# Kernel optimization log

Hardware: AMD Instinct MI355X
Metric: run time of the kernel (lower is better)

The kernel has to match this reference:

```python
import jax, jax.numpy as jnp
import numpy as np

B, H, N, P = 2, 8, 2048, 64   # batch, heads, seq, head_dim
M, D = 4, 256                 # sketch count, sketch feature dim


def setup_inputs() -> dict:
    key = jax.random.key(0)
    kq, kk, ks, kr = jax.random.split(key, 4)
    scale = P ** -0.5  # keep exp(QK) numerically tame, std(dot) ~= 1/8
    Q = jax.random.normal(kq, (B, H, N, P), dtype=jnp.float32) * scale
    K = jax.random.normal(kk, (B, H, N, P), dtype=jnp.float32) * scale
    # indices into the concatenated [Q;K] token axis of length 2N
    sketching_matrix = jax.random.randint(ks, (B, M, D), 0, 2 * N)
    # Rademacher random signs, broadcast over [b,h,2n] in the reduction
    random_sign = jnp.sign(jax.random.normal(kr, (M, D), dtype=jnp.float32))
    random_sign = jnp.where(random_sign == 0, 1.0, random_sign)
    return {"Q": Q, "K": K, "sketching_matrix": sketching_matrix,
            "random_sign": random_sign}


def reference(Q, K, sketching_matrix, random_sign):
    b, h, n, p = Q.shape
    X = jnp.concatenate([Q, K], axis=2)          # [b,h,2n,p]
    Xt = jnp.transpose(X, (0, 2, 1, 3))          # [b,2n,h,p]
    # gather sketched landmarks: [b,m,d,h,p] -> [b,h,m,d,p]
    XS = Xt[jnp.arange(b)[:, None, None], sketching_matrix]
    XS = jnp.transpose(XS, (0, 3, 1, 2, 4))
    # RS_SM accumulate branch: exp of inner products, random-sign reduce over m
    product = jnp.einsum('bhnp,bhmdp->bhnmd', X, XS)   # [b,h,2n,m,d]
    AS = jnp.einsum('bhnmd,md->bhnd', jnp.exp(product), random_sign)
    return AS.astype(Q.dtype)                    # [b,h,2n,d]
```

## Files before the change

### kernel.cpp

```cpp
#include <hip/hip_runtime.h>
#include <hip/hip_bf16.h>

typedef __attribute__((ext_vector_type(8))) short short8;
typedef __attribute__((ext_vector_type(4))) float f32x4;

namespace {
constexpr int Hc  = 8;
constexpr int Nc  = 2048;
constexpr int NXc = 4096;
constexpr int Pc  = 64;
constexpr int Mc  = 4;
constexpr int Dc  = 256;
constexpr int TN  = 128;
constexpr int LDX = 72;
constexpr int DCk = 64;
}

__device__ inline unsigned int bfpack(float a, float b) {
  union { __hip_bfloat162 h; unsigned int u; } cv;
  cv.h = __float22bfloat162_rn(make_float2(a, b));
  return cv.u;
}

__global__ __launch_bounds__(256, 2) void sketch_kernel(
    const float* __restrict__ Q, const float* __restrict__ K,
    const int* __restrict__ SK, const float* __restrict__ SGN,
    float* __restrict__ OUT)
{
  __shared__ __hip_bfloat16 Xs[TN][LDX];
  __shared__ __hip_bfloat16 Ws[DCk][LDX];
  __shared__ float Ss[Mc * Dc];

  const int t    = threadIdx.x;
  const int lane = t & 63;
  const int wv   = t >> 6;
  const int bh   = blockIdx.y;
  const int b    = bh >> 3;
  const int n0   = blockIdx.x * TN;

  for (int i = t; i < Mc * Dc; i += 256) Ss[i] = SGN[i];

  {
    const int q  = t & 3;
    const int r0 = t >> 2;
    for (int half = 0; half < 2; ++half) {
      const int r = r0 + half * 64;
      const int n = n0 + r;
      const float* src = (n < Nc) ? (Q + ((size_t)bh * Nc + n) * Pc)
                                  : (K + ((size_t)bh * Nc + (n - Nc)) * Pc);
      const f32x4* s4 = (const f32x4*)(src + q * 16);
      f32x4 f0 = s4[0], f1 = s4[1], f2 = s4[2], f3 = s4[3];
      uint4 u, v;
      u.x = bfpack(f0.x, f0.y); u.y = bfpack(f0.z, f0.w);
      u.z = bfpack(f1.x, f1.y); u.w = bfpack(f1.z, f1.w);
      v.x = bfpack(f2.x, f2.y); v.y = bfpack(f2.z, f2.w);
      v.z = bfpack(f3.x, f3.y); v.w = bfpack(f3.z, f3.w);
      *(uint4*)&Xs[r][q * 16]     = u;
      *(uint4*)&Xs[r][q * 16 + 8] = v;
    }
  }

  __syncthreads();

  short8 afr[2][2];
  const int acol = (lane >> 4) * 8;
  {
    const int arow = wv * 32 + (lane & 15);
    for (int ti = 0; ti < 2; ++ti)
      for (int ks = 0; ks < 2; ++ks)
        afr[ti][ks] = *(const short8*)&Xs[arow + ti * 16][ks * 32 + acol];
  }

  for (int dc = 0; dc < 4; ++dc) {
    f32x4 AS[2][4];
    for (int ti = 0; ti < 2; ++ti)
      for (int tj = 0; tj < 4; ++tj)
        AS[ti][tj] = (f32x4){0.f, 0.f, 0.f, 0.f};

    for (int m = 0; m < Mc; ++m) {
      __syncthreads();
      {
        const int q = t & 3;
        const int r = t >> 2;
        const int d = dc * 64 + r;
        const int idx = SK[b * (Mc * Dc) + m * Dc + d];
        const float* src = (idx < Nc) ? (Q + ((size_t)bh * Nc + idx) * Pc)
                                      : (K + ((size_t)bh * Nc + (idx - Nc)) * Pc);
        const f32x4* s4 = (const f32x4*)(src + q * 16);
        f32x4 f0 = s4[0], f1 = s4[1], f2 = s4[2], f3 = s4[3];
        uint4 u, v;
        u.x = bfpack(f0.x, f0.y); u.y = bfpack(f0.z, f0.w);
        u.z = bfpack(f1.x, f1.y); u.w = bfpack(f1.z, f1.w);
        v.x = bfpack(f2.x, f2.y); v.y = bfpack(f2.z, f2.w);
        v.z = bfpack(f3.x, f3.y); v.w = bfpack(f3.z, f3.w);
        *(uint4*)&Ws[r][q * 16]     = u;
        *(uint4*)&Ws[r][q * 16 + 8] = v;
      }
      __syncthreads();

      short8 bfr[4][2];
      const int brow = lane & 15;
      for (int tj = 0; tj < 4; ++tj)
        for (int ks = 0; ks < 2; ++ks)
          bfr[tj][ks] = *(const short8*)&Ws[tj * 16 + brow][ks * 32 + acol];

      for (int ti = 0; ti < 2; ++ti)
        for (int tj = 0; tj < 4; ++tj) {
          f32x4 c = {0.f, 0.f, 0.f, 0.f};
          c = __builtin_amdgcn_mfma_f32_16x16x32_bf16(afr[ti][0], bfr[tj][0], c, 0, 0, 0);
          c = __builtin_amdgcn_mfma_f32_16x16x32_bf16(afr[ti][1], bfr[tj][1], c, 0, 0, 0);
          const float sg = Ss[m * Dc + dc * 64 + tj * 16 + (lane & 15)];
          AS[ti][tj].x += sg * __expf(c.x);
          AS[ti][tj].y += sg * __expf(c.y);
          AS[ti][tj].z += sg * __expf(c.z);
          AS[ti][tj].w += sg * __expf(c.w);
        }
    }

    const int dbase = dc * 64 + (lane & 15);
    const int nb    = n0 + wv * 32 + ((lane >> 4) << 2);
    for (int ti = 0; ti < 2; ++ti)
      for (int tj = 0; tj < 4; ++tj) {
        const size_t base = ((size_t)bh * NXc + (nb + ti * 16)) * Dc + dbase + tj * 16;
        OUT[base + 0 * (size_t)Dc] = AS[ti][tj].x;
        OUT[base + 1 * (size_t)Dc] = AS[ti][tj].y;
        OUT[base + 2 * (size_t)Dc] = AS[ti][tj].z;
        OUT[base + 3 * (size_t)Dc] = AS[ti][tj].w;
      }
  }
}

extern "C" void kernel_launch(void* const* d_in, const int* in_sizes, int n_in,
                              void* d_out, int out_size, void* d_ws, size_t ws_size,
                              hipStream_t stream) {
  (void)in_sizes; (void)n_in; (void)out_size; (void)d_ws; (void)ws_size;
  const float* Q   = (const float*)d_in[0];
  const float* K   = (const float*)d_in[1];
  const int*   SK  = (const int*)d_in[2];
  const float* SGN = (const float*)d_in[3];
  float* OUT = (float*)d_out;

  dim3 grid(NXc / TN, 16);
  dim3 block(256);
  sketch_kernel<<<grid, block, 0, stream>>>(Q, K, SK, SGN, OUT);
}
```

Measured before the change: 105.0 us.

## Split into bf16 prepass plus double-buffered MFMA main kernel with exp2

A prepass kernel converts Q/K rows and the gathered sketch landmarks to bf16 once into workspace, folding log2(e) into the landmark rows so the main kernel can use a hardware exp2. This removes the repeated fp32 gather and convert work each block did before. The main kernel uses smaller 64-row tiles for more blocks and higher occupancy, double-buffers the landmark tile in shared memory with register prefetch, and walks a flattened 16-step (dc, m) loop. It adds a second launch and a workspace round-trip, and scaling before the bf16 rounding slightly changes the numerics.

Result: faster. 102.3 us (-2.6%).

```diff
diff --git a/kernel.cpp b/kernel.cpp
--- a/kernel.cpp
+++ b/kernel.cpp
@@ -5,15 +5,22 @@
 typedef __attribute__((ext_vector_type(4))) float f32x4;
 
 namespace {
-constexpr int Hc  = 8;
 constexpr int Nc  = 2048;
 constexpr int NXc = 4096;
 constexpr int Pc  = 64;
 constexpr int Mc  = 4;
 constexpr int Dc  = 256;
-constexpr int TN  = 128;
-constexpr int LDX = 72;
-constexpr int DCk = 64;
+constexpr int BH  = 16;
+constexpr int LDW = 72;
+constexpr float LOG2E = 1.4426950408889634f;
+}
+
+__device__ inline float fexp2(float x) {
+#if __has_builtin(__builtin_amdgcn_exp2f)
+  return __builtin_amdgcn_exp2f(x);
+#else
+  return exp2f(x);
+#endif
 }
 
 __device__ inline unsigned int bfpack(float a, float b) {
@@ -22,125 +29,146 @@
   return cv.u;
 }
 
-__global__ __launch_bounds__(256, 2) void sketch_kernel(
+__global__ __launch_bounds__(256) void prepass_kernel(
     const float* __restrict__ Q, const float* __restrict__ K,
-    const int* __restrict__ SK, const float* __restrict__ SGN,
-    float* __restrict__ OUT)
+    const int* __restrict__ SK,
+    __hip_bfloat16* __restrict__ Xb, __hip_bfloat16* __restrict__ Wb)
 {
-  __shared__ __hip_bfloat16 Xs[TN][LDX];
-  __shared__ __hip_bfloat16 Ws[DCk][LDX];
+  const int t = blockIdx.x * 256 + threadIdx.x;
+  const int q = t & 7;
+  const int r = t >> 3;
+  const int NXROWS = BH * NXc;
+
+  const float* src;
+  __hip_bfloat16* dst;
+  float scale;
+  if (r < NXROWS) {
+    const int bh = r >> 12, n = r & (NXc - 1);
+    src = (n < Nc) ? (Q + ((size_t)bh * Nc + n) * Pc)
+                   : (K + ((size_t)bh * Nc + (n - Nc)) * Pc);
+    dst = Xb + (size_t)r * Pc;
+    scale = 1.0f;
+  } else {
+    const int j  = r - NXROWS;
+    const int bh = j >> 10;
+    const int md = j & 1023;
+    const int b  = bh >> 3;
+    const int idx = SK[b * (Mc * Dc) + md];
+    src = (idx < Nc) ? (Q + ((size_t)bh * Nc + idx) * Pc)
+                     : (K + ((size_t)bh * Nc + (idx - Nc)) * Pc);
+    dst = Wb + (size_t)j * Pc;
+    scale = LOG2E;
+  }
+  const f32x4* s4 = (const f32x4*)(src + q * 8);
+  f32x4 f0 = s4[0], f1 = s4[1];
+  uint4 u;
+  u.x = bfpack(f0.x * scale, f0.y * scale);
+  u.y = bfpack(f0.z * scale, f0.w * scale);
+  u.z = bfpack(f1.x * scale, f1.y * scale);
+  u.w = bfpack(f1.z * scale, f1.w * scale);
+  *(uint4*)(dst + q * 8) = u;
+}
+
+__global__ __launch_bounds__(256, 4) void sketch_main(
+    const __hip_bfloat16* __restrict__ Xb, const __hip_bfloat16* __restrict__ Wb,
+    const float* __restrict__ SGN, float* __restrict__ OUT)
+{
+  __shared__ __hip_bfloat16 Ws[2][64][LDW];
   __shared__ float Ss[Mc * Dc];
 
   const int t    = threadIdx.x;
   const int lane = t & 63;
   const int wv   = t >> 6;
   const int bh   = blockIdx.y;
-  const int b    = bh >> 3;
-  const int n0   = blockIdx.x * TN;
+  const int n0   = blockIdx.x * 64;
 
   for (int i = t; i < Mc * Dc; i += 256) Ss[i] = SGN[i];
 
+  const int brow = lane & 15;
+  const int acol = (lane >> 4) * 8;
+  short8 afr[2];
   {
-    const int q  = t & 3;
-    const int r0 = t >> 2;
-    for (int half = 0; half < 2; ++half) {
-      const int r = r0 + half * 64;
-      const int n = n0 + r;
-      const float* src = (n < Nc) ? (Q + ((size_t)bh * Nc + n) * Pc)
-                                  : (K + ((size_t)bh * Nc + (n - Nc)) * Pc);
-      const f32x4* s4 = (const f32x4*)(src + q * 16);
-      f32x4 f0 = s4[0], f1 = s4[1], f2 = s4[2], f3 = s4[3];
-      uint4 u, v;
-      u.x = bfpack(f0.x, f0.y); u.y = bfpack(f0.z, f0.w);
-      u.z = bfpack(f1.x, f1.y); u.w = bfpack(f1.z, f1.w);
-      v.x = bfpack(f2.x, f2.y); v.y = bfpack(f2.z, f2.w);
-      v.z = bfpack(f3.x, f3.y); v.w = bfpack(f3.z, f3.w);
-      *(uint4*)&Xs[r][q * 16]     = u;
-      *(uint4*)&Xs[r][q * 16 + 8] = v;
-    }
+    const __hip_bfloat16* ap =
+        Xb + ((size_t)bh * NXc + n0 + wv * 16 + brow) * Pc + acol;
+    afr[0] = *(const short8*)ap;
+    afr[1] = *(const short8*)(ap + 32);
   }
 
+  const __hip_bfloat16* wbase = Wb + (size_t)bh * (Mc * Dc) * Pc;
+  const int tr = t >> 2;
+  const int tq = t & 3;
+
+  auto crow = [](int p) { return (p & 3) * Dc + (p >> 2) * 64; };
+
+  {
+    const __hip_bfloat16* wp = wbase + (size_t)(crow(0) + tr) * Pc + tq * 16;
+    uint4 wa = *(const uint4*)wp;
+    uint4 wb = *(const uint4*)(wp + 8);
+    *(uint4*)&Ws[0][tr][tq * 16]     = wa;
+    *(uint4*)&Ws[0][tr][tq * 16 + 8] = wb;
+  }
   __syncthreads();
 
-  short8 afr[2][2];
-  const int acol = (lane >> 4) * 8;
-  {
-    const int arow = wv * 32 + (lane & 15);
-    for (int ti = 0; ti < 2; ++ti)
-      for (int ks = 0; ks < 2; ++ks)
-        afr[ti][ks] = *(const short8*)&Xs[arow + ti * 16][ks * 32 + acol];
-  }
+  f32x4 AS[4];
+  for (int tj = 0; tj < 4; ++tj) AS[tj] = (f32x4){0.f, 0.f, 0.f, 0.f};
 
-  for (int dc = 0; dc < 4; ++dc) {
-    f32x4 AS[2][4];
-    for (int ti = 0; ti < 2; ++ti)
-      for (int tj = 0; tj < 4; ++tj)
-        AS[ti][tj] = (f32x4){0.f, 0.f, 0.f, 0.f};
+  for (int p = 0; p < 16; ++p) {
+    const int pn = (p < 15) ? p + 1 : 15;
+    const __hip_bfloat16* wp = wbase + (size_t)(crow(pn) + tr) * Pc + tq * 16;
+    uint4 wa = *(const uint4*)wp;
+    uint4 wb = *(const uint4*)(wp + 8);
 
-    for (int m = 0; m < Mc; ++m) {
-      __syncthreads();
-      {
-        const int q = t & 3;
-        const int r = t >> 2;
-        const int d = dc * 64 + r;
-        const int idx = SK[b * (Mc * Dc) + m * Dc + d];
-        const float* src = (idx < Nc) ? (Q + ((size_t)bh * Nc + idx) * Pc)
-                                      : (K + ((size_t)bh * Nc + (idx - Nc)) * Pc);
-        const f32x4* s4 = (const f32x4*)(src + q * 16);
-        f32x4 f0 = s4[0], f1 = s4[1], f2 = s4[2], f3 = s4[3];
-        uint4 u, v;
-        u.x = bfpack(f0.x, f0.y); u.y = bfpack(f0.z, f0.w);
-        u.z = bfpack(f1.x, f1.y); u.w = bfpack(f1.z, f1.w);
-        v.x = bfpack(f2.x, f2.y); v.y = bfpack(f2.z, f2.w);
-        v.z = bfpack(f3.x, f3.y); v.w = bfpack(f3.z, f3.w);
-        *(uint4*)&Ws[r][q * 16]     = u;
-        *(uint4*)&Ws[r][q * 16 + 8] = v;
-      }
-      __syncthreads();
-
-      short8 bfr[4][2];
-      const int brow = lane & 15;
-      for (int tj = 0; tj < 4; ++tj)
-        for (int ks = 0; ks < 2; ++ks)
-          bfr[tj][ks] = *(const short8*)&Ws[tj * 16 + brow][ks * 32 + acol];
-
-      for (int ti = 0; ti < 2; ++ti)
-        for (int tj = 0; tj < 4; ++tj) {
-          f32x4 c = {0.f, 0.f, 0.f, 0.f};
-          c = __builtin_amdgcn_mfma_f32_16x16x32_bf16(afr[ti][0], bfr[tj][0], c, 0, 0, 0);
-          c = __builtin_amdgcn_mfma_f32_16x16x32_bf16(afr[ti][1], bfr[tj][1], c, 0, 0, 0);
-          const float sg = Ss[m * Dc + dc * 64 + tj * 16 + (lane & 15)];
-          AS[ti][tj].x += sg * __expf(c.x);
-          AS[ti][tj].y += sg * __expf(c.y);
-          AS[ti][tj].z += sg * __expf(c.z);
-          AS[ti][tj].w += sg * __expf(c.w);
-        }
+    const int buf = p & 1;
+    short8 bfr[4][2];
+    for (int tj = 0; tj < 4; ++tj) {
+      bfr[tj][0] = *(const short8*)&Ws[buf][tj * 16 + brow][acol];
+      bfr[tj][1] = *(const short8*)&Ws[buf][tj * 16 + brow][32 + acol];
+    }
+    const int m  = p & 3;
+    const int dc = p >> 2;
+    for (int tj = 0; tj < 4; ++tj) {
+      f32x4 c = {0.f, 0.f, 0.f, 0.f};
+      c = __builtin_amdgcn_mfma_f32_16x16x32_bf16(afr[0], bfr[tj][0], c, 0, 0, 0);
+      c = __builtin_amdgcn_mfma_f32_16x16x32_bf16(afr[1], bfr[tj][1], c, 0, 0, 0);
+      const float sg = Ss[m * Dc + dc * 64 + tj * 16 + brow];
+      AS[tj].x = fmaf(sg, fexp2(c.x), AS[tj].x);
+      AS[tj].y = fmaf(sg, fexp2(c.y), AS[tj].y);
+      AS[tj].z = fmaf(sg, fexp2(c.z), AS[tj].z);
+      AS[tj].w = fmaf(sg, fexp2(c.w), AS[tj].w);
     }
 
-    const int dbase = dc * 64 + (lane & 15);
-    const int nb    = n0 + wv * 32 + ((lane >> 4) << 2);
-    for (int ti = 0; ti < 2; ++ti)
+    if (m == 3) {
+      const int nb    = n0 + wv * 16 + ((lane >> 4) << 2);
+      const int dbase = dc * 64 + brow;
       for (int tj = 0; tj < 4; ++tj) {
-        const size_t base = ((size_t)bh * NXc + (nb + ti * 16)) * Dc + dbase + tj * 16;
-        OUT[base + 0 * (size_t)Dc] = AS[ti][tj].x;
-        OUT[base + 1 * (size_t)Dc] = AS[ti][tj].y;
-        OUT[base + 2 * (size_t)Dc] = AS[ti][tj].z;
-        OUT[base + 3 * (size_t)Dc] = AS[ti][tj].w;
+        const size_t base = ((size_t)bh * NXc + nb) * Dc + dbase + tj * 16;
+        OUT[base + 0 * (size_t)Dc] = AS[tj].x;
+        OUT[base + 1 * (size_t)Dc] = AS[tj].y;
+        OUT[base + 2 * (size_t)Dc] = AS[tj].z;
+        OUT[base + 3 * (size_t)Dc] = AS[tj].w;
+        AS[tj] = (f32x4){0.f, 0.f, 0.f, 0.f};
       }
+    }
+
+    *(uint4*)&Ws[buf ^ 1][tr][tq * 16]     = wa;
+    *(uint4*)&Ws[buf ^ 1][tr][tq * 16 + 8] = wb;
+    __syncthreads();
   }
 }
 
 extern "C" void kernel_launch(void* const* d_in, const int* in_sizes, int n_in,
                               void* d_out, int out_size, void* d_ws, size_t ws_size,
                               hipStream_t stream) {
-  (void)in_sizes; (void)n_in; (void)out_size; (void)d_ws; (void)ws_size;
+  (void)in_sizes; (void)n_in; (void)out_size; (void)ws_size;
   const float* Q   = (const float*)d_in[0];
   const float* K   = (const float*)d_in[1];
   const int*   SK  = (const int*)d_in[2];
   const float* SGN = (const float*)d_in[3];
   float* OUT = (float*)d_out;
 
-  dim3 grid(NXc / TN, 16);
-  dim3 block(256);
-  sketch_kernel<<<grid, block, 0, stream>>>(Q, K, SK, SGN, OUT);
+  __hip_bfloat16* Xb = (__hip_bfloat16*)d_ws;
+  __hip_bfloat16* Wb = (__hip_bfloat16*)((char*)d_ws + (size_t)BH * NXc * Pc * 2);
+
+  prepass_kernel<<<dim3(2560), dim3(256), 0, stream>>>(Q, K, SK, Xb, Wb);
+  sketch_main<<<dim3(NXc / 64, BH), dim3(256), 0, stream>>>(Xb, Wb, SGN, OUT);
 }
```
